# Optimization experiments

Hardware: AMD Instinct MI355X
Metric: run time of the kernel (lower is better)

## Reference

```python
import jax, jax.numpy as jnp
import numpy as np

B, CIN, COUT, H, W = 16, 512, 128, 64, 64


def setup_inputs() -> dict:
    key = jax.random.key(0)
    k1, k2, k3 = jax.random.split(key, 3)
    x = jax.random.normal(k1, (B, CIN, H, W), dtype=jnp.float32)
    style = jax.random.normal(k2, (B, CIN), dtype=jnp.float32)
    # kaiming_normal_ on [COUT, CIN, 1, 1]: fan_in = CIN*1*1, std = sqrt(2/fan_in)
    weight = jax.random.normal(k3, (COUT, CIN), dtype=jnp.float32) * np.float32(np.sqrt(2.0 / CIN))
    return {"x": x, "style": style, "weight": weight}


def reference(x, style, weight):
    # Per-sample modulated weight: mw[b,o,c] = style[b,c] * weight[o,c]
    # 1x1 conv, padding=0, stride=1 -> batched channel-mixing GEMM:
    # out[b,o,h,w] = sum_c mw[b,o,c] * x[b,c,h,w]
    return jnp.einsum('oc,bc,bchw->bohw', weight, style, x)
```

## Files before the change

kernel.cpp:

```cpp
#include <hip/hip_runtime.h>

#define NB    16
#define CIN   512
#define COUT  128
#define HW    4096
#define BN    64
#define BK    32
#define NIT   (CIN / BK)
#define NTILES (HW / BN)

using bf16x8  = __attribute__((ext_vector_type(8))) __bf16;
using floatx4 = __attribute__((ext_vector_type(4))) float;

__device__ __forceinline__ unsigned short f2bf_bits(float f) {
    union { float f; unsigned u; } v; v.f = f;
    return (unsigned short)((v.u + 0x7fffu + ((v.u >> 16) & 1u)) >> 16);
}

__global__ __launch_bounds__(256, 4)
void modconv1x1_kernel(const float* __restrict__ x,
                       const float* __restrict__ style,
                       const float* __restrict__ weight,
                       float* __restrict__ out)
{
    __shared__ __align__(16) __bf16 Alds[2][(BK / 8) * COUT * 8];
    __shared__ __align__(16) __bf16 Blds[2][(BK / 8) * BN * 8];
    __shared__ float style_s[CIN];

    const int tid = threadIdx.x;
    const int b   = blockIdx.x >> 6;
    const int n0  = (blockIdx.x & 63) * BN;

    const float* xb   = x   + (size_t)b * CIN * HW + n0;
    float*       outb = out + (size_t)b * COUT * HW + n0;

    style_s[tid]       = style[b * CIN + tid];
    style_s[tid + 256] = style[b * CIN + tid + 256];

    const int lane = tid & 63;
    const int wave = tid >> 6;
    const int quad = lane >> 4;
    const int l15  = lane & 15;
    const int wm   = (wave & 1) * 64;
    const int wn   = (wave >> 1) * 32;

    const int am  = tid >> 2;
    const int ak8 = tid & 3;
    const int bn_ = lane;
    const int bk8 = wave;

    floatx4 acc[4][2];
    #pragma unroll
    for (int i = 0; i < 4; ++i)
        #pragma unroll
        for (int j = 0; j < 2; ++j)
            acc[i][j] = (floatx4){0.f, 0.f, 0.f, 0.f};

    float4 ra[2][2];
    float  rb[8];

#define LOAD_TILE(K0)                                                          \
    {                                                                          \
        const int kb = (K0) + ak8 * 8;                                         \
        _Pragma("unroll")                                                      \
        for (int i = 0; i < 2; ++i) {                                          \
            ra[i][0] = *(const float4*)(weight + (am + 64 * i) * CIN + kb);    \
            ra[i][1] = *(const float4*)(weight + (am + 64 * i) * CIN + kb + 4);\
        }                                                                      \
        const float* src = xb + (size_t)((K0) + bk8 * 8) * HW + bn_;           \
        _Pragma("unroll")                                                      \
        for (int j = 0; j < 8; ++j)                                            \
            rb[j] = src[(size_t)j * HW];                                       \
    }

#define WRITE_TILE(BUF, K0)                                                    \
    {                                                                          \
        const int kb = (K0) + ak8 * 8;                                         \
        _Pragma("unroll")                                                      \
        for (int i = 0; i < 2; ++i) {                                          \
            const float* rap = (const float*)&ra[i][0];                        \
            union { unsigned short us[8]; bf16x8 v; } pk;                      \
            _Pragma("unroll")                                                  \
            for (int j = 0; j < 8; ++j)                                        \
                pk.us[j] = f2bf_bits(rap[j] * style_s[kb + j]);                \
            const int unit = 128 * ak8 + ((am + 64 * i) ^ (ak8 << 1));         \
            *(bf16x8*)&Alds[BUF][unit * 8] = pk.v;                             \
        }                                                                      \
        union { unsigned short us[8]; bf16x8 v; } pb;                          \
        _Pragma("unroll")                                                      \
        for (int j = 0; j < 8; ++j)                                            \
            pb.us[j] = f2bf_bits(rb[j]);                                       \
        *(bf16x8*)&Blds[BUF][(64 * bk8 + bn_) * 8] = pb.v;                     \
    }

    __syncthreads();

    LOAD_TILE(0)
    WRITE_TILE(0, 0)

    int cur = 0;
    for (int it = 0; it < NIT; ++it) {
        const int knext = (it + 1) * BK;
        __syncthreads();
        if (it + 1 < NIT) LOAD_TILE(knext)

        bf16x8 af[4], bfr[2];
        #pragma unroll
        for (int tm = 0; tm < 4; ++tm) {
            const int unit = 128 * quad + ((wm + tm * 16 + l15) ^ (quad << 1));
            af[tm] = *(const bf16x8*)&Alds[cur][unit * 8];
        }
        #pragma unroll
        for (int tn = 0; tn < 2; ++tn)
            bfr[tn] = *(const bf16x8*)&Blds[cur][(64 * quad + wn + tn * 16 + l15) * 8];
        #pragma unroll
        for (int tm = 0; tm < 4; ++tm)
            #pragma unroll
            for (int tn = 0; tn < 2; ++tn)
                acc[tm][tn] = __builtin_amdgcn_mfma_f32_16x16x32_bf16(
                    af[tm], bfr[tn], acc[tm][tn], 0, 0, 0);

        if (it + 1 < NIT) WRITE_TILE(cur ^ 1, knext)
        cur ^= 1;
    }

    #pragma unroll
    for (int tm = 0; tm < 4; ++tm) {
        const int o = wm + tm * 16 + quad * 4;
        #pragma unroll
        for (int tn = 0; tn < 2; ++tn) {
            const int n = wn + tn * 16 + l15;
            #pragma unroll
            for (int r = 0; r < 4; ++r)
                outb[(size_t)(o + r) * HW + n] = acc[tm][tn][r];
        }
    }
#undef LOAD_TILE
#undef WRITE_TILE
}

extern "C" void kernel_launch(void* const* d_in, const int* in_sizes, int n_in,
                              void* d_out, int out_size, void* d_ws, size_t ws_size,
                              hipStream_t stream) {
    const float* x      = (const float*)d_in[0];
    const float* style  = (const float*)d_in[1];
    const float* weight = (const float*)d_in[2];
    float* out = (float*)d_out;

    modconv1x1_kernel<<<dim3(NB * NTILES), dim3(256), 0, stream>>>(x, style, weight, out);
}
```

Measured before the change: 218.9 us.

## Precompute modulated bf16 weights and stream them to LDS via global_load_lds

Adds a small pre-kernel that multiplies style by weight per sample, converts to bf16, and writes the result to workspace in the LDS tile layout. The main GEMM kernel then copies A tiles straight into LDS with global_load_lds instead of loading fp32 weights, scaling and converting them in every block. This removes redundant per-block modulation work and register staging for A. In exchange it adds a second launch and workspace traffic, and drops the XOR swizzle on A reads, which may introduce LDS bank conflicts.

```diff
diff --git a/kernel.cpp b/kernel.cpp
--- a/kernel.cpp
+++ b/kernel.cpp
@@ -1,4 +1,5 @@
 #include <hip/hip_runtime.h>
+#include <stdint.h>
 
 #define NB    16
 #define CIN   512
@@ -17,15 +18,45 @@
     return (unsigned short)((v.u + 0x7fffu + ((v.u >> 16) & 1u)) >> 16);
 }
 
+#define GLD16(g, l)                                                            \
+    __builtin_amdgcn_global_load_lds(                                          \
+        (const __attribute__((address_space(1))) void*)(g),                    \
+        (__attribute__((address_space(3))) void*)(l), 16, 0, 0)
+
+__global__ __launch_bounds__(256)
+void modw_kernel(const float* __restrict__ style,
+                 const float* __restrict__ weight,
+                 __bf16* __restrict__ mw)
+{
+    const int id = blockIdx.x * 256 + threadIdx.x;
+    const int k8 = id & 63;
+    const int m  = (id >> 6) & 127;
+    const int b  = id >> 13;
+
+    const float4 w0 = *(const float4*)(weight + m * CIN + k8 * 8);
+    const float4 w1 = *(const float4*)(weight + m * CIN + k8 * 8 + 4);
+    const float4 s0 = *(const float4*)(style + b * CIN + k8 * 8);
+    const float4 s1 = *(const float4*)(style + b * CIN + k8 * 8 + 4);
+
+    union { unsigned short us[8]; bf16x8 v; } pk;
+    pk.us[0] = f2bf_bits(w0.x * s0.x);
+    pk.us[1] = f2bf_bits(w0.y * s0.y);
+    pk.us[2] = f2bf_bits(w0.z * s0.z);
+    pk.us[3] = f2bf_bits(w0.w * s0.w);
+    pk.us[4] = f2bf_bits(w1.x * s1.x);
+    pk.us[5] = f2bf_bits(w1.y * s1.y);
+    pk.us[6] = f2bf_bits(w1.z * s1.z);
+    pk.us[7] = f2bf_bits(w1.w * s1.w);
+    *(bf16x8*)(mw + ((size_t)(b * 64 + k8) * 128 + m) * 8) = pk.v;
+}
+
 __global__ __launch_bounds__(256, 4)
 void modconv1x1_kernel(const float* __restrict__ x,
-                       const float* __restrict__ style,
-                       const float* __restrict__ weight,
+                       const __bf16* __restrict__ mw,
                        float* __restrict__ out)
 {
     __shared__ __align__(16) __bf16 Alds[2][(BK / 8) * COUT * 8];
     __shared__ __align__(16) __bf16 Blds[2][(BK / 8) * BN * 8];
-    __shared__ float style_s[CIN];
 
     const int tid = threadIdx.x;
     const int b   = blockIdx.x >> 6;
@@ -33,9 +64,7 @@
 
     const float* xb   = x   + (size_t)b * CIN * HW + n0;
     float*       outb = out + (size_t)b * COUT * HW + n0;
-
-    style_s[tid]       = style[b * CIN + tid];
-    style_s[tid + 256] = style[b * CIN + tid + 256];
+    const char*  mwb  = (const char*)mw + (size_t)b * (64 * 128 * 16);
 
     const int lane = tid & 63;
     const int wave = tid >> 6;
@@ -44,8 +73,6 @@
     const int wm   = (wave & 1) * 64;
     const int wn   = (wave >> 1) * 32;
 
-    const int am  = tid >> 2;
-    const int ak8 = tid & 3;
     const int bn_ = lane;
     const int bk8 = wave;
 
@@ -56,63 +83,45 @@
         for (int j = 0; j < 2; ++j)
             acc[i][j] = (floatx4){0.f, 0.f, 0.f, 0.f};
 
-    float4 ra[2][2];
-    float  rb[8];
+    {
+        const char* t  = mwb;
+        char*       al = (char*)&Alds[0][0];
+        GLD16(t + wave * 2048 + lane * 16,        al + wave * 2048);
+        GLD16(t + wave * 2048 + 1024 + lane * 16, al + wave * 2048 + 1024);
 
-#define LOAD_TILE(K0)                                                          \
-    {                                                                          \
-        const int kb = (K0) + ak8 * 8;                                         \
-        _Pragma("unroll")                                                      \
-        for (int i = 0; i < 2; ++i) {                                          \
-            ra[i][0] = *(const float4*)(weight + (am + 64 * i) * CIN + kb);    \
-            ra[i][1] = *(const float4*)(weight + (am + 64 * i) * CIN + kb + 4);\
-        }                                                                      \
-        const float* src = xb + (size_t)((K0) + bk8 * 8) * HW + bn_;           \
-        _Pragma("unroll")                                                      \
-        for (int j = 0; j < 8; ++j)                                            \
-            rb[j] = src[(size_t)j * HW];                                       \
+        const float* src = xb + (size_t)(bk8 * 8) * HW + bn_;
+        float rb[8];
+        #pragma unroll
+        for (int j = 0; j < 8; ++j) rb[j] = src[(size_t)j * HW];
+        union { unsigned short us[8]; bf16x8 v; } pk;
+        #pragma unroll
+        for (int j = 0; j < 8; ++j) pk.us[j] = f2bf_bits(rb[j]);
+        *(bf16x8*)&Blds[0][(bk8 * BN + bn_) * 8] = pk.v;
     }
-
-#define WRITE_TILE(BUF, K0)                                                    \
-    {                                                                          \
-        const int kb = (K0) + ak8 * 8;                                         \
-        _Pragma("unroll")                                                      \
-        for (int i = 0; i < 2; ++i) {                                          \
-            const float* rap = (const float*)&ra[i][0];                        \
-            union { unsigned short us[8]; bf16x8 v; } pk;                      \
-            _Pragma("unroll")                                                  \
-            for (int j = 0; j < 8; ++j)                                        \
-                pk.us[j] = f2bf_bits(rap[j] * style_s[kb + j]);                \
-            const int unit = 128 * ak8 + ((am + 64 * i) ^ (ak8 << 1));         \
-            *(bf16x8*)&Alds[BUF][unit * 8] = pk.v;                             \
-        }                                                                      \
-        union { unsigned short us[8]; bf16x8 v; } pb;                          \
-        _Pragma("unroll")                                                      \
-        for (int j = 0; j < 8; ++j)                                            \
-            pb.us[j] = f2bf_bits(rb[j]);                                       \
-        *(bf16x8*)&Blds[BUF][(64 * bk8 + bn_) * 8] = pb.v;                     \
-    }
-
-    __syncthreads();
-
-    LOAD_TILE(0)
-    WRITE_TILE(0, 0)
 
     int cur = 0;
     for (int it = 0; it < NIT; ++it) {
-        const int knext = (it + 1) * BK;
         __syncthreads();
-        if (it + 1 < NIT) LOAD_TILE(knext)
+
+        float rb[8];
+        if (it + 1 < NIT) {
+            const int knext = (it + 1) * BK;
+            const char* t  = mwb + (size_t)knext * 256;
+            char*       al = (char*)&Alds[cur ^ 1][0];
+            GLD16(t + wave * 2048 + lane * 16,        al + wave * 2048);
+            GLD16(t + wave * 2048 + 1024 + lane * 16, al + wave * 2048 + 1024);
+            const float* src = xb + (size_t)(knext + bk8 * 8) * HW + bn_;
+            #pragma unroll
+            for (int j = 0; j < 8; ++j) rb[j] = src[(size_t)j * HW];
+        }
 
         bf16x8 af[4], bfr[2];
         #pragma unroll
-        for (int tm = 0; tm < 4; ++tm) {
-            const int unit = 128 * quad + ((wm + tm * 16 + l15) ^ (quad << 1));
-            af[tm] = *(const bf16x8*)&Alds[cur][unit * 8];
-        }
+        for (int tm = 0; tm < 4; ++tm)
+            af[tm] = *(const bf16x8*)&Alds[cur][(quad * COUT + wm + tm * 16 + l15) * 8];
         #pragma unroll
         for (int tn = 0; tn < 2; ++tn)
-            bfr[tn] = *(const bf16x8*)&Blds[cur][(64 * quad + wn + tn * 16 + l15) * 8];
+            bfr[tn] = *(const bf16x8*)&Blds[cur][(quad * BN + wn + tn * 16 + l15) * 8];
         #pragma unroll
         for (int tm = 0; tm < 4; ++tm)
             #pragma unroll
@@ -120,7 +129,12 @@
                 acc[tm][tn] = __builtin_amdgcn_mfma_f32_16x16x32_bf16(
                     af[tm], bfr[tn], acc[tm][tn], 0, 0, 0);
 
-        if (it + 1 < NIT) WRITE_TILE(cur ^ 1, knext)
+        if (it + 1 < NIT) {
+            union { unsigned short us[8]; bf16x8 v; } pk;
+            #pragma unroll
+            for (int j = 0; j < 8; ++j) pk.us[j] = f2bf_bits(rb[j]);
+            *(bf16x8*)&Blds[cur ^ 1][(bk8 * BN + bn_) * 8] = pk.v;
+        }
         cur ^= 1;
     }
 
@@ -135,8 +149,6 @@
                 outb[(size_t)(o + r) * HW + n] = acc[tm][tn][r];
         }
     }
-#undef LOAD_TILE
-#undef WRITE_TILE
 }
 
 extern "C" void kernel_launch(void* const* d_in, const int* in_sizes, int n_in,
@@ -146,6 +158,8 @@
     const float* style  = (const float*)d_in[1];
     const float* weight = (const float*)d_in[2];
     float* out = (float*)d_out;
+    __bf16* mw = (__bf16*)d_ws;
 
-    modconv1x1_kernel<<<dim3(NB * NTILES), dim3(256), 0, stream>>>(x, style, weight, out);
+    modw_kernel<<<dim3(512), dim3(256), 0, stream>>>(style, weight, mw);
+    modconv1x1_kernel<<<dim3(NB * NTILES), dim3(256), 0, stream>>>(x, mw, out);
 }
```

New measurement: 213.0 us. 1.03x faster.
